# Kernel tuning notes

Hardware: AMD Instinct MI355X
Metric: run time of the kernel (lower is better)

## Reference

```python
import jax, jax.numpy as jnp
import numpy as np

N = 8192
K = 15


def setup_inputs() -> dict:
    key = jax.random.key(0)
    kx, ky = jax.random.split(key)
    x = jax.random.normal(kx, (N, 2), dtype=jnp.float32)
    y = jax.random.randint(ky, (N,), 0, 2, dtype=jnp.int32)
    return {"x": x, "y": y}


def reference(x, y):
    # Pairwise squared Euclidean distances via ||a||^2 + ||b||^2 - 2 a.b
    n = x.shape[0]
    xx = jnp.sum(x * x, axis=-1)                      # [n]
    d = xx[:, None] + xx[None, :] - 2.0 * (x @ x.T)   # [n, n]
    # exclude self (the original loop skips i == j)
    idx = jnp.arange(n)
    d = d.at[idx, idx].set(jnp.inf)
    # K nearest neighbors per point (smallest distances)
    _, knn_idx = jax.lax.top_k(-d, K)                 # [n, K]
    knn_labels = y[knn_idx].astype(jnp.float32)       # [n, K]
    # majority vote: sum of K binary labels > K/2 -> class 1
    out = (jnp.sum(knn_labels, axis=-1) > (K / 2)).astype(jnp.float32)
    return out
```

## Files before the change

### kernel.cpp

```cpp
#include <hip/hip_runtime.h>
#include <hip/hip_fp16.h>

#define NPTS 8192
#define KNN  15
#define WPB  8
#define TPB  (WPB * 64)
#define SEG  64

__device__ __forceinline__ int prefix_below(unsigned long long m) {
  return (int)__builtin_amdgcn_mbcnt_hi((unsigned int)(m >> 32),
            __builtin_amdgcn_mbcnt_lo((unsigned int)m, 0u));
}

__device__ __forceinline__ __half2 hmin2(__half2 a, __half2 b) {
  __half2 r;
  asm("v_pk_min_f16 %0, %1, %2" : "=v"(r) : "v"(a), "v"(b));
  return r;
}

__device__ __forceinline__ unsigned int bitonic_sort_u32(unsigned int v, int lane) {
#pragma unroll
  for (int k = 2; k <= 64; k <<= 1) {
#pragma unroll
    for (int j = k >> 1; j > 0; j >>= 1) {
      unsigned int o = __shfl_xor(v, j, 64);
      bool keep_min = ((lane & k) == 0) == ((lane & j) == 0);
      unsigned int lo = (v < o) ? v : o;
      unsigned int hi = (v < o) ? o : v;
      v = keep_min ? lo : hi;
    }
  }
  return v;
}

__device__ __forceinline__ unsigned long long bitonic_sort_u64(unsigned long long v, int lane) {
#pragma unroll
  for (int k = 2; k <= 64; k <<= 1) {
#pragma unroll
    for (int j = k >> 1; j > 0; j >>= 1) {
      unsigned long long o = __shfl_xor(v, j, 64);
      bool keep_min = ((lane & k) == 0) == ((lane & j) == 0);
      unsigned long long lo = (v < o) ? v : o;
      unsigned long long hi = (v < o) ? o : v;
      v = keep_min ? lo : hi;
    }
  }
  return v;
}

__global__ __launch_bounds__(TPB)
void knn_kernel(const float* __restrict__ x, const int* __restrict__ y,
                float* __restrict__ out) {
  __shared__ __align__(16) unsigned int sp[NPTS];
  __shared__ unsigned int ybits[NPTS / 32];
  __shared__ unsigned int buf[WPB][SEG];

  const int tid = threadIdx.x;

  const float4* gx4 = (const float4*)x;
#pragma unroll
  for (int i = tid; i < NPTS / 2; i += TPB) {
    float4 p = gx4[i];
    __half2 hx = __floats2half2_rn(p.x, p.z);
    __half2 hy = __floats2half2_rn(p.y, p.w);
    sp[2 * i]     = *(const unsigned int*)&hx;
    sp[2 * i + 1] = *(const unsigned int*)&hy;
  }
  if (tid < NPTS / 32) {
    const int4* yy = (const int4*)(y + (tid << 5));
    unsigned int b = 0;
#pragma unroll
    for (int k2 = 0; k2 < 8; ++k2) {
      int4 v = yy[k2];
      b |= ((unsigned int)(v.x & 1) << (4 * k2)) |
           ((unsigned int)(v.y & 1) << (4 * k2 + 1)) |
           ((unsigned int)(v.z & 1) << (4 * k2 + 2)) |
           ((unsigned int)(v.w & 1) << (4 * k2 + 3));
    }
    ybits[tid] = b;
  }
  __syncthreads();

  const int w = tid >> 6;
  const int lane = tid & 63;
  const int q = (int)blockIdx.x * WPB + w;
  const float2 xq = ((const float2*)x)[q];
  const __half2 qx2 = __floats2half2_rn(xq.x, xq.x);
  const __half2 qy2 = __floats2half2_rn(xq.y, xq.y);

  const uint4* sp4 = (const uint4*)sp;

  __half2 mm = __floats2half2_rn(6.0e4f, 6.0e4f);
#pragma unroll 4
  for (int s = 0; s < 32; ++s) {
    uint4 v = sp4[(s << 6) + lane];
    __half2 xa = *(const __half2*)&v.x, ya = *(const __half2*)&v.y;
    __half2 xb = *(const __half2*)&v.z, yb = *(const __half2*)&v.w;
    __half2 dxa = __hsub2(xa, qx2), dya = __hsub2(ya, qy2);
    __half2 dxb = __hsub2(xb, qx2), dyb = __hsub2(yb, qy2);
    __half2 da = __hfma2(dxa, dxa, __hmul2(dya, dya));
    __half2 db = __hfma2(dxb, dxb, __hmul2(dyb, dyb));
    mm = hmin2(mm, hmin2(da, db));
  }
  float m = fminf(__low2float(mm), __high2float(mm));

  unsigned int srt = bitonic_sort_u32(__float_as_uint(m), lane);
  const float T = __uint_as_float(__shfl(srt, KNN, 64));
  const float M = 0.035f * sqrtf(T) + 2.0e-4f + 0.01f * T;
  __half hTf = __float2half_rn(T + M);
  hTf = __ushort_as_half((unsigned short)(__half_as_ushort(hTf) + 2));
  const __half2 Tf2 = __half2half2(hTf);

  int cnt = 0;
#pragma unroll 2
  for (int s = 0; s < 32; ++s) {
    uint4 v = sp4[(s << 6) + lane];
    __half2 xa = *(const __half2*)&v.x, ya = *(const __half2*)&v.y;
    __half2 xb = *(const __half2*)&v.z, yb = *(const __half2*)&v.w;
    __half2 dxa = __hsub2(xa, qx2), dya = __hsub2(ya, qy2);
    __half2 dxb = __hsub2(xb, qx2), dyb = __hsub2(yb, qy2);
    __half2 da = __hfma2(dxa, dxa, __hmul2(dya, dya));
    __half2 db = __hfma2(dxb, dxb, __hmul2(dyb, dyb));
    __half2 ta = __hsub2(Tf2, da);
    __half2 tb = __hsub2(Tf2, db);
    unsigned int sa = *(const unsigned int*)&ta;
    unsigned int sb = *(const unsigned int*)&tb;
    if (__any((sa & sb & 0x80008000u) != 0x80008000u)) {
      int jb = ((s << 6) + lane) << 2;
      bool c0 = (sa & 0x00008000u) == 0;
      bool c1 = (sa & 0x80000000u) == 0;
      bool c2 = (sb & 0x00008000u) == 0;
      bool c3 = (sb & 0x80000000u) == 0;
      unsigned long long k0 = __ballot(c0);
      if (c0) { int o = cnt + prefix_below(k0); if (o < SEG) buf[w][o] = jb; }
      cnt += __popcll(k0);
      unsigned long long k1 = __ballot(c1);
      if (c1) { int o = cnt + prefix_below(k1); if (o < SEG) buf[w][o] = jb + 1; }
      cnt += __popcll(k1);
      unsigned long long k2 = __ballot(c2);
      if (c2) { int o = cnt + prefix_below(k2); if (o < SEG) buf[w][o] = jb + 2; }
      cnt += __popcll(k2);
      unsigned long long k3 = __ballot(c3);
      if (c3) { int o = cnt + prefix_below(k3); if (o < SEG) buf[w][o] = jb + 3; }
      cnt += __popcll(k3);
    }
  }

  int C = (cnt > SEG) ? SEG : cnt;
  unsigned long long kv = ~0ull;
  if (lane < C) {
    int jj = (int)buf[w][lane];
    float2 pj = ((const float2*)x)[jj];
    double dx = (double)xq.x - (double)pj.x;
    double dy = (double)xq.y - (double)pj.y;
    double dd = dx * dx + dy * dy;
    kv = ((unsigned long long)__double_as_longlong(dd) & ~0x1FFFull) |
         (unsigned long long)jj;
    if (jj == q) kv = ~0ull;
  }
  kv = bitonic_sort_u64(kv, lane);
  int j15 = (int)(kv & 0x1FFFull);
  int lbl = (int)((ybits[j15 >> 5] >> (j15 & 31)) & 1u);
  unsigned long long vm = __ballot((lane < KNN) && lbl);
  if (lane == 0) out[q] = (__popcll(vm) >= 8) ? 1.0f : 0.0f;
}

extern "C" void kernel_launch(void* const* d_in, const int* in_sizes, int n_in,
                              void* d_out, int out_size, void* d_ws, size_t ws_size,
                              hipStream_t stream) {
  const float* x = (const float*)d_in[0];
  const int* y = (const int*)d_in[1];
  float* out = (float*)d_out;
  dim3 grid(NPTS / WPB);
  dim3 block(TPB);
  hipLaunchKernelGGL(knn_kernel, grid, block, 0, stream, x, y, out);
}
```

Before: 32.31 us.

## Process two queries per wavefront to reuse shared-memory point loads

Each wavefront now handles two query points, so every LDS load of packed candidate coordinates serves both distance computations in the bound and the filter passes. The grid is halved, which also halves the per-block cost of staging all points and labels into shared memory. A per-wave XOR offset on the segment index staggers which LDS segment different waves read first. The trade-off is more registers per thread, fewer blocks to spread across CUs, and a longer serial filter and sort phase per wave.

Result: slower. 35.25 us (+9.1%).

```diff
diff --git a/kernel.cpp b/kernel.cpp
--- a/kernel.cpp
+++ b/kernel.cpp
@@ -3,6 +3,7 @@
 
 #define NPTS 8192
 #define KNN  15
+#define QPW  2
 #define WPB  8
 #define TPB  (WPB * 64)
 #define SEG  64
@@ -53,7 +54,7 @@
                 float* __restrict__ out) {
   __shared__ __align__(16) unsigned int sp[NPTS];
   __shared__ unsigned int ybits[NPTS / 32];
-  __shared__ unsigned int buf[WPB][SEG];
+  __shared__ unsigned int buf[WPB][QPW][SEG];
 
   const int tid = threadIdx.x;
 
@@ -83,86 +84,146 @@
 
   const int w = tid >> 6;
   const int lane = tid & 63;
-  const int q = (int)blockIdx.x * WPB + w;
-  const float2 xq = ((const float2*)x)[q];
-  const __half2 qx2 = __floats2half2_rn(xq.x, xq.x);
-  const __half2 qy2 = __floats2half2_rn(xq.y, xq.y);
+  const int q0 = ((int)blockIdx.x * WPB + w) * QPW;
+  const float2 xqa = ((const float2*)x)[q0];
+  const float2 xqb = ((const float2*)x)[q0 + 1];
+  const __half2 qxa = __floats2half2_rn(xqa.x, xqa.x);
+  const __half2 qya = __floats2half2_rn(xqa.y, xqa.y);
+  const __half2 qxb = __floats2half2_rn(xqb.x, xqb.x);
+  const __half2 qyb = __floats2half2_rn(xqb.y, xqb.y);
 
   const uint4* sp4 = (const uint4*)sp;
-
-  __half2 mm = __floats2half2_rn(6.0e4f, 6.0e4f);
+  const int off = ((w << 2) | ((int)blockIdx.x & 3)) & 31;
+
+  __half2 mma = __floats2half2_rn(6.0e4f, 6.0e4f);
+  __half2 mmb = mma;
 #pragma unroll 4
   for (int s = 0; s < 32; ++s) {
-    uint4 v = sp4[(s << 6) + lane];
-    __half2 xa = *(const __half2*)&v.x, ya = *(const __half2*)&v.y;
-    __half2 xb = *(const __half2*)&v.z, yb = *(const __half2*)&v.w;
-    __half2 dxa = __hsub2(xa, qx2), dya = __hsub2(ya, qy2);
-    __half2 dxb = __hsub2(xb, qx2), dyb = __hsub2(yb, qy2);
-    __half2 da = __hfma2(dxa, dxa, __hmul2(dya, dya));
-    __half2 db = __hfma2(dxb, dxb, __hmul2(dyb, dyb));
-    mm = hmin2(mm, hmin2(da, db));
-  }
-  float m = fminf(__low2float(mm), __high2float(mm));
-
-  unsigned int srt = bitonic_sort_u32(__float_as_uint(m), lane);
-  const float T = __uint_as_float(__shfl(srt, KNN, 64));
-  const float M = 0.035f * sqrtf(T) + 2.0e-4f + 0.01f * T;
-  __half hTf = __float2half_rn(T + M);
-  hTf = __ushort_as_half((unsigned short)(__half_as_ushort(hTf) + 2));
-  const __half2 Tf2 = __half2half2(hTf);
-
-  int cnt = 0;
+    uint4 v = sp4[((s ^ off) << 6) + lane];
+    __half2 px0 = *(const __half2*)&v.x, py0 = *(const __half2*)&v.y;
+    __half2 px1 = *(const __half2*)&v.z, py1 = *(const __half2*)&v.w;
+    __half2 adx0 = __hsub2(px0, qxa), ady0 = __hsub2(py0, qya);
+    __half2 adx1 = __hsub2(px1, qxa), ady1 = __hsub2(py1, qya);
+    __half2 da0 = __hfma2(adx0, adx0, __hmul2(ady0, ady0));
+    __half2 da1 = __hfma2(adx1, adx1, __hmul2(ady1, ady1));
+    mma = hmin2(mma, hmin2(da0, da1));
+    __half2 bdx0 = __hsub2(px0, qxb), bdy0 = __hsub2(py0, qyb);
+    __half2 bdx1 = __hsub2(px1, qxb), bdy1 = __hsub2(py1, qyb);
+    __half2 db0 = __hfma2(bdx0, bdx0, __hmul2(bdy0, bdy0));
+    __half2 db1 = __hfma2(bdx1, bdx1, __hmul2(bdy1, bdy1));
+    mmb = hmin2(mmb, hmin2(db0, db1));
+  }
+
+  __half2 Tf2a, Tf2b;
+  {
+    float m = fminf(__low2float(mma), __high2float(mma));
+    unsigned int srt = bitonic_sort_u32(__float_as_uint(m), lane);
+    const float T = __uint_as_float(__shfl(srt, KNN, 64));
+    const float M = 0.035f * sqrtf(T) + 2.0e-4f + 0.01f * T;
+    __half hT = __float2half_rn(T + M);
+    hT = __ushort_as_half((unsigned short)(__half_as_ushort(hT) + 2));
+    Tf2a = __half2half2(hT);
+  }
+  {
+    float m = fminf(__low2float(mmb), __high2float(mmb));
+    unsigned int srt = bitonic_sort_u32(__float_as_uint(m), lane);
+    const float T = __uint_as_float(__shfl(srt, KNN, 64));
+    const float M = 0.035f * sqrtf(T) + 2.0e-4f + 0.01f * T;
+    __half hT = __float2half_rn(T + M);
+    hT = __ushort_as_half((unsigned short)(__half_as_ushort(hT) + 2));
+    Tf2b = __half2half2(hT);
+  }
+
+  int cA = 0, cB = 0;
 #pragma unroll 2
   for (int s = 0; s < 32; ++s) {
-    uint4 v = sp4[(s << 6) + lane];
-    __half2 xa = *(const __half2*)&v.x, ya = *(const __half2*)&v.y;
-    __half2 xb = *(const __half2*)&v.z, yb = *(const __half2*)&v.w;
-    __half2 dxa = __hsub2(xa, qx2), dya = __hsub2(ya, qy2);
-    __half2 dxb = __hsub2(xb, qx2), dyb = __hsub2(yb, qy2);
-    __half2 da = __hfma2(dxa, dxa, __hmul2(dya, dya));
-    __half2 db = __hfma2(dxb, dxb, __hmul2(dyb, dyb));
-    __half2 ta = __hsub2(Tf2, da);
-    __half2 tb = __hsub2(Tf2, db);
-    unsigned int sa = *(const unsigned int*)&ta;
-    unsigned int sb = *(const unsigned int*)&tb;
-    if (__any((sa & sb & 0x80008000u) != 0x80008000u)) {
-      int jb = ((s << 6) + lane) << 2;
-      bool c0 = (sa & 0x00008000u) == 0;
-      bool c1 = (sa & 0x80000000u) == 0;
-      bool c2 = (sb & 0x00008000u) == 0;
-      bool c3 = (sb & 0x80000000u) == 0;
-      unsigned long long k0 = __ballot(c0);
-      if (c0) { int o = cnt + prefix_below(k0); if (o < SEG) buf[w][o] = jb; }
-      cnt += __popcll(k0);
-      unsigned long long k1 = __ballot(c1);
-      if (c1) { int o = cnt + prefix_below(k1); if (o < SEG) buf[w][o] = jb + 1; }
-      cnt += __popcll(k1);
-      unsigned long long k2 = __ballot(c2);
-      if (c2) { int o = cnt + prefix_below(k2); if (o < SEG) buf[w][o] = jb + 2; }
-      cnt += __popcll(k2);
-      unsigned long long k3 = __ballot(c3);
-      if (c3) { int o = cnt + prefix_below(k3); if (o < SEG) buf[w][o] = jb + 3; }
-      cnt += __popcll(k3);
-    }
-  }
-
-  int C = (cnt > SEG) ? SEG : cnt;
-  unsigned long long kv = ~0ull;
-  if (lane < C) {
-    int jj = (int)buf[w][lane];
-    float2 pj = ((const float2*)x)[jj];
-    double dx = (double)xq.x - (double)pj.x;
-    double dy = (double)xq.y - (double)pj.y;
-    double dd = dx * dx + dy * dy;
-    kv = ((unsigned long long)__double_as_longlong(dd) & ~0x1FFFull) |
-         (unsigned long long)jj;
-    if (jj == q) kv = ~0ull;
-  }
-  kv = bitonic_sort_u64(kv, lane);
-  int j15 = (int)(kv & 0x1FFFull);
-  int lbl = (int)((ybits[j15 >> 5] >> (j15 & 31)) & 1u);
-  unsigned long long vm = __ballot((lane < KNN) && lbl);
-  if (lane == 0) out[q] = (__popcll(vm) >= 8) ? 1.0f : 0.0f;
+    const int si = s ^ off;
+    uint4 v = sp4[(si << 6) + lane];
+    __half2 px0 = *(const __half2*)&v.x, py0 = *(const __half2*)&v.y;
+    __half2 px1 = *(const __half2*)&v.z, py1 = *(const __half2*)&v.w;
+    const int jb = (si << 8) + (lane << 2);
+
+    {
+      __half2 dx0 = __hsub2(px0, qxa), dy0 = __hsub2(py0, qya);
+      __half2 dx1 = __hsub2(px1, qxa), dy1 = __hsub2(py1, qya);
+      __half2 d0 = __hfma2(dx0, dx0, __hmul2(dy0, dy0));
+      __half2 d1 = __hfma2(dx1, dx1, __hmul2(dy1, dy1));
+      __half2 t0 = __hsub2(Tf2a, d0);
+      __half2 t1 = __hsub2(Tf2a, d1);
+      unsigned int s0 = *(const unsigned int*)&t0;
+      unsigned int s1 = *(const unsigned int*)&t1;
+      if (__any((s0 & s1 & 0x80008000u) != 0x80008000u)) {
+        bool c0 = (s0 & 0x00008000u) == 0;
+        bool c1 = (s0 & 0x80000000u) == 0;
+        bool c2 = (s1 & 0x00008000u) == 0;
+        bool c3 = (s1 & 0x80000000u) == 0;
+        unsigned long long k0 = __ballot(c0);
+        if (c0) { int o = cA + prefix_below(k0); if (o < SEG) buf[w][0][o] = jb; }
+        cA += __popcll(k0);
+        unsigned long long k1 = __ballot(c1);
+        if (c1) { int o = cA + prefix_below(k1); if (o < SEG) buf[w][0][o] = jb + 1; }
+        cA += __popcll(k1);
+        unsigned long long k2 = __ballot(c2);
+        if (c2) { int o = cA + prefix_below(k2); if (o < SEG) buf[w][0][o] = jb + 2; }
+        cA += __popcll(k2);
+        unsigned long long k3 = __ballot(c3);
+        if (c3) { int o = cA + prefix_below(k3); if (o < SEG) buf[w][0][o] = jb + 3; }
+        cA += __popcll(k3);
+      }
+    }
+    {
+      __half2 dx0 = __hsub2(px0, qxb), dy0 = __hsub2(py0, qyb);
+      __half2 dx1 = __hsub2(px1, qxb), dy1 = __hsub2(py1, qyb);
+      __half2 d0 = __hfma2(dx0, dx0, __hmul2(dy0, dy0));
+      __half2 d1 = __hfma2(dx1, dx1, __hmul2(dy1, dy1));
+      __half2 t0 = __hsub2(Tf2b, d0);
+      __half2 t1 = __hsub2(Tf2b, d1);
+      unsigned int s0 = *(const unsigned int*)&t0;
+      unsigned int s1 = *(const unsigned int*)&t1;
+      if (__any((s0 & s1 & 0x80008000u) != 0x80008000u)) {
+        bool c0 = (s0 & 0x00008000u) == 0;
+        bool c1 = (s0 & 0x80000000u) == 0;
+        bool c2 = (s1 & 0x00008000u) == 0;
+        bool c3 = (s1 & 0x80000000u) == 0;
+        unsigned long long k0 = __ballot(c0);
+        if (c0) { int o = cB + prefix_below(k0); if (o < SEG) buf[w][1][o] = jb; }
+        cB += __popcll(k0);
+        unsigned long long k1 = __ballot(c1);
+        if (c1) { int o = cB + prefix_below(k1); if (o < SEG) buf[w][1][o] = jb + 1; }
+        cB += __popcll(k1);
+        unsigned long long k2 = __ballot(c2);
+        if (c2) { int o = cB + prefix_below(k2); if (o < SEG) buf[w][1][o] = jb + 2; }
+        cB += __popcll(k2);
+        unsigned long long k3 = __ballot(c3);
+        if (c3) { int o = cB + prefix_below(k3); if (o < SEG) buf[w][1][o] = jb + 3; }
+        cB += __popcll(k3);
+      }
+    }
+  }
+
+#pragma unroll
+  for (int qi = 0; qi < QPW; ++qi) {
+    const int q = q0 + qi;
+    const float2 xq = (qi == 0) ? xqa : xqb;
+    int C = (qi == 0) ? cA : cB;
+    C = (C > SEG) ? SEG : C;
+    unsigned long long kv = ~0ull;
+    if (lane < C) {
+      int jj = (int)buf[w][qi][lane];
+      float2 pj = ((const float2*)x)[jj];
+      double dx = (double)xq.x - (double)pj.x;
+      double dy = (double)xq.y - (double)pj.y;
+      double dd = dx * dx + dy * dy;
+      kv = ((unsigned long long)__double_as_longlong(dd) & ~0x1FFFull) |
+           (unsigned long long)jj;
+      if (jj == q) kv = ~0ull;
+    }
+    kv = bitonic_sort_u64(kv, lane);
+    int j15 = (int)(kv & 0x1FFFull);
+    int lbl = (int)((ybits[j15 >> 5] >> (j15 & 31)) & 1u);
+    unsigned long long vm = __ballot((lane < KNN) && lbl);
+    if (lane == 0) out[q] = (__popcll(vm) >= 8) ? 1.0f : 0.0f;
+  }
 }
 
 extern "C" void kernel_launch(void* const* d_in, const int* in_sizes, int n_in,
@@ -171,7 +232,7 @@
   const float* x = (const float*)d_in[0];
   const int* y = (const int*)d_in[1];
   float* out = (float*)d_out;
-  dim3 grid(NPTS / WPB);
+  dim3 grid(NPTS / (WPB * QPW));
   dim3 block(TPB);
   hipLaunchKernelGGL(knn_kernel, grid, block, 0, stream, x, y, out);
 }
```
